# Kernel optimization log

Hardware: AMD Instinct MI355X
Metric: run time of the kernel (lower is better)

## Reference

```python
import jax, jax.numpy as jnp
import numpy as np

K = 512
H = 8

def setup_inputs() -> dict:
    key = jax.random.key(0)
    k1, k2, k3, k4, k5 = jax.random.split(key, 5)
    b, s = 2, 2048
    x = jax.random.normal(k1, (b, s, K), dtype=jnp.float32)
    # torch Linear weights: shape [out_features, in_features]
    scale = 0.02
    Wq = jax.random.normal(k2, (H * K, K), dtype=jnp.float32) * scale
    Wk = jax.random.normal(k3, (H * K, K), dtype=jnp.float32) * scale
    Wv = jax.random.normal(k4, (H * K, K), dtype=jnp.float32) * scale
    Wu = jax.random.normal(k5, (K, H * K), dtype=jnp.float32) * scale
    return {"x": x, "Wq": Wq, "Wk": Wk, "Wv": Wv, "Wu": Wu}

def reference(x, Wq, Wk, Wv, Wu):
    b, s, _ = x.shape
    # project and split heads: [b, h, s, k]
    q = jnp.einsum('bsd,hed->bhse', x, Wq.reshape(H, K, K))
    kk = jnp.einsum('bsd,hed->bhse', x, Wk.reshape(H, K, K))
    v = jnp.einsum('bsd,hed->bhse', x, Wv.reshape(H, K, K))
    scale = K ** (-0.25)
    dot = jnp.einsum('bhse,bhte->bhst', q * scale, kk * scale)  # [b,h,s,s]
    causal = jnp.tril(jnp.ones((s, s), dtype=bool))
    dot = jnp.where(causal[None, None], dot, -jnp.inf)
    weights = jax.nn.softmax(dot, axis=-1)
    heads_out = jnp.einsum('bhst,bhte->bhse', weights, v)  # [b,h,s,k]
    heads_out = heads_out.transpose(0, 2, 1, 3).reshape(b, s, H * K)
    return heads_out @ Wu.T
```

## Files before the change

### kernel.cpp

```cpp
#include <hip/hip_runtime.h>
#include <hip/hip_bf16.h>
#include <cstdint>
#include <cstddef>


typedef __bf16 bf16;
typedef __bf16 bf16x8 __attribute__((ext_vector_type(8)));
typedef float  f32x4  __attribute__((ext_vector_type(4)));
typedef unsigned short u16x4 __attribute__((ext_vector_type(4)));

__device__ __forceinline__ void gl2lds16(const void* g, void* l) {
  __builtin_amdgcn_global_load_lds(
      (const __attribute__((address_space(1))) unsigned int*)g,
      (__attribute__((address_space(3))) unsigned int*)l, 16, 0, 0);
}

__device__ __forceinline__ unsigned short bfbits(float f) {
  return __builtin_bit_cast(unsigned short, (__bf16)f);
}

__global__ __launch_bounds__(256) void cvt_all(
    const float* __restrict__ x,  const float* __restrict__ wq,
    const float* __restrict__ wk, const float* __restrict__ wv,
    const float* __restrict__ wu,
    bf16* __restrict__ xb,  bf16* __restrict__ wqb, bf16* __restrict__ wkb,
    bf16* __restrict__ wvb, bf16* __restrict__ wub)
{
  const int Q4 = (1 << 21) / 4;
  int i = blockIdx.x * 256 + threadIdx.x;
  int a = i / Q4;
  int off = (i - a * Q4) * 4;
  const float* s; bf16* d;
  switch (a) {
    case 0: s = x;  d = xb;  break;
    case 1: s = wq; d = wqb; break;
    case 2: s = wk; d = wkb; break;
    case 3: s = wv; d = wvb; break;
    default: s = wu; d = wub; break;
  }
  float4 v = *(const float4*)(s + off);
  u16x4 o = { bfbits(v.x), bfbits(v.y), bfbits(v.z), bfbits(v.w) };
  *(u16x4*)(d + off) = o;
}

template<int BM, int BN, int MODE>
__global__ __launch_bounds__((BM >= 256 ? 2 : BM / 64) * (BN / 64) * 64)
void gemm_bt(const bf16* __restrict__ A, const bf16* __restrict__ B,
             void* __restrict__ Cp, int M, int N, int K)
{
  constexpr int BK = 32;
  constexpr int WM = (BM >= 256 ? 128 : 64);
  constexpr int MI = WM / 16;
  constexpr int WAVES_M = BM / WM;
  constexpr int WAVES_N = BN / 64;
  constexpr int NT = WAVES_M * WAVES_N * 64;
  constexpr int STG = 2 * (BM + BN) * BK;
  constexpr int EPE = (MODE == 0) ? 128 * 264
                    : (MODE == 1) ? 256 * 136
                    : 64 * 132 * 2;
  constexpr int SME = STG > EPE ? STG : EPE;
  __shared__ __align__(16) bf16 smem[SME];

  const int tid = threadIdx.x, w = tid >> 6, lane = tid & 63;
  const int g = lane >> 4, c16 = lane & 15;
  const int q8 = gridDim.x >> 3;
  const int wg = (blockIdx.x & 7) * q8 + (blockIdx.x >> 3);
  const int nbn = N / BN;
  const int bm = wg / nbn, bn = wg % nbn;
  const int m0 = bm * BM, n0 = bn * BN;
  const int wr = w / WAVES_N, wc = w % WAVES_N;

  f32x4 z = {0.f, 0.f, 0.f, 0.f};
  f32x4 acc[MI][4];
  #pragma unroll
  for (int i = 0; i < MI; i++)
    #pragma unroll
    for (int j = 0; j < 4; j++) acc[i][j] = z;

  const int nk = K / BK;

  auto stage = [&](int buf, int kt) {
    bf16* la = &smem[buf * (BM + BN) * BK];
    #pragma unroll
    for (int r = 0; r < (BM * BK / 8) / NT; r++) {
      int c = r * NT + tid;
      int row = c >> 2, p = c & 3, s = p ^ ((row >> 1) & 3);
      gl2lds16(A + (size_t)(m0 + row) * K + (size_t)kt * BK + s * 8,
               la + (r * NT + w * 64) * 8);
    }
    bf16* lb = &smem[buf * (BM + BN) * BK + BM * BK];
    #pragma unroll
    for (int r = 0; r < (BN * BK / 8) / NT; r++) {
      int c = r * NT + tid;
      int row = c >> 2, p = c & 3, s = p ^ ((row >> 1) & 3);
      gl2lds16(B + (size_t)(n0 + row) * K + (size_t)kt * BK + s * 8,
               lb + (r * NT + w * 64) * 8);
    }
  };

  stage(0, 0);
  __syncthreads();
  int cur = 0;
  for (int kt = 0; kt < nk; ++kt) {
    if (kt + 1 < nk) stage(cur ^ 1, kt + 1);
    const bf16* lA = &smem[cur * (BM + BN) * BK];
    const bf16* lB = &smem[cur * (BM + BN) * BK + BM * BK];
    bf16x8 af[MI], bfv[4];
    #pragma unroll
    for (int i = 0; i < MI; i++) {
      int ra = wr * WM + i * 16 + c16;
      af[i] = *(const bf16x8*)&lA[ra * BK + ((g ^ ((ra >> 1) & 3)) * 8)];
    }
    #pragma unroll
    for (int j = 0; j < 4; j++) {
      int rb = wc * 64 + j * 16 + c16;
      bfv[j] = *(const bf16x8*)&lB[rb * BK + ((g ^ ((rb >> 1) & 3)) * 8)];
    }
    #pragma unroll
    for (int i = 0; i < MI; i++)
      #pragma unroll
      for (int j = 0; j < 4; j++)
        acc[i][j] = __builtin_amdgcn_mfma_f32_16x16x32_bf16(af[i], bfv[j],
                                                            acc[i][j], 0, 0, 0);
    __syncthreads();
    cur ^= 1;
  }

  if constexpr (MODE == 0) {
    bf16* ep = smem;
    #pragma unroll
    for (int hp = 0; hp < 2; ++hp) {
      if (wr == hp) {
        #pragma unroll
        for (int i = 0; i < MI; i++) {
          int rl = i * 16 + g * 4;
          #pragma unroll
          for (int j = 0; j < 4; j++) {
            int cl = wc * 64 + j * 16 + c16;
            #pragma unroll
            for (int jj = 0; jj < 4; jj++)
              ep[(rl + jj) * 264 + cl] = (bf16)acc[i][j][jj];
          }
        }
      }
      __syncthreads();
      {
        bf16* C = (bf16*)Cp;
        int r = tid >> 2, ch = tid & 3;
        const bf16* src = &ep[r * 264 + ch * 64];
        bf16* dst = C + (size_t)(m0 + hp * 128 + r) * N + n0 + ch * 64;
        #pragma unroll
        for (int q = 0; q < 8; q++)
          *(bf16x8*)(dst + q * 8) = *(const bf16x8*)(src + q * 8);
      }
      if (hp == 0) __syncthreads();
    }
  } else if constexpr (MODE == 1) {
    bf16* ep = smem;
    bf16* C = (bf16*)Cp;
    #pragma unroll
    for (int hp = 0; hp < 2; ++hp) {
      if (wr == hp) {
        #pragma unroll
        for (int i = 0; i < MI; i++) {
          int rl = i * 16 + g * 4;
          #pragma unroll
          for (int j = 0; j < 4; j++) {
            int cl = wc * 64 + j * 16 + c16;
            u16x4 pk = { bfbits(acc[i][j][0]), bfbits(acc[i][j][1]),
                         bfbits(acc[i][j][2]), bfbits(acc[i][j][3]) };
            *(u16x4*)&ep[cl * 136 + rl] = pk;
          }
        }
      }
      __syncthreads();
      {
        int cl = tid >> 1, rc = tid & 1;
        const bf16* src = &ep[cl * 136 + rc * 64];
        int mg = m0 + hp * 128 + rc * 64;
        int bb = mg >> 11, srow = mg & 2047;
        bf16* dst = C + ((size_t)(bb * 4096 + n0 + cl)) * 2048 + srow;
        #pragma unroll
        for (int q = 0; q < 8; q++)
          *(bf16x8*)(dst + q * 8) = *(const bf16x8*)(src + q * 8);
      }
      if (hp == 0) __syncthreads();
    }
  } else {
    float* ep = (float*)smem;
    #pragma unroll
    for (int i = 0; i < MI; i++) {
      int rl = i * 16 + g * 4;
      #pragma unroll
      for (int j = 0; j < 4; j++) {
        int cl = wc * 64 + j * 16 + c16;
        #pragma unroll
        for (int jj = 0; jj < 4; jj++)
          ep[(rl + jj) * 132 + cl] = acc[i][j][jj];
      }
    }
    __syncthreads();
    {
      float* C = (float*)Cp;
      int r = tid >> 1, ch = tid & 1;
      const float* src = &ep[r * 132 + ch * 64];
      float* dst = C + (size_t)(m0 + r) * N + n0 + ch * 64;
      #pragma unroll
      for (int q = 0; q < 16; q++)
        *(float4*)(dst + q * 4) = *(const float4*)(src + q * 4);
    }
  }
}

__global__ __launch_bounds__(512)
void sgemm_causal(const bf16* __restrict__ Qb, const bf16* __restrict__ Kb,
                  bf16* __restrict__ Sp, float* __restrict__ l)
{
  constexpr int BK = 32;
  constexpr int STG = 2 * 512 * BK;
  constexpr int EPE = 128 * 264;
  __shared__ __align__(16) bf16 smem[EPE > STG ? EPE : STG];
  const int tid = threadIdx.x, w = tid >> 6, lane = tid & 63;
  const int g = lane >> 4, c16 = lane & 15;

  const int wg = (blockIdx.x & 7) * 72 + (blockIdx.x >> 3);
  const int bh = wg / 36, t = wg % 36;
  int TM = 0;
  while ((TM + 1) * (TM + 2) / 2 <= t) TM++;
  const int TN = t - TM * (TM + 1) / 2;
  const int b = bh >> 3, h = bh & 7;
  const bf16* Ab = Qb + (size_t)(b * 2048 + TM * 256) * 4096 + h * 512;
  const bf16* Bb = Kb + (size_t)(b * 2048 + TN * 256) * 4096 + h * 512;
  const int wr = w >> 2, wc = w & 3;

  f32x4 z = {0.f, 0.f, 0.f, 0.f};
  f32x4 acc[8][4];
  #pragma unroll
  for (int i = 0; i < 8; i++)
    #pragma unroll
    for (int j = 0; j < 4; j++) acc[i][j] = z;

  auto stage = [&](int buf, int kt) {
    bf16* la = &smem[buf * 16384];
    #pragma unroll
    for (int r = 0; r < 2; r++) {
      int c = r * 512 + tid;
      int row = c >> 2, p = c & 3, s = p ^ ((row >> 1) & 3);
      gl2lds16(Ab + (size_t)row * 4096 + kt * BK + s * 8,
               la + (r * 512 + w * 64) * 8);
    }
    bf16* lb = &smem[buf * 16384 + 256 * BK];
    #pragma unroll
    for (int r = 0; r < 2; r++) {
      int c = r * 512 + tid;
      int row = c >> 2, p = c & 3, s = p ^ ((row >> 1) & 3);
      gl2lds16(Bb + (size_t)row * 4096 + kt * BK + s * 8,
               lb + (r * 512 + w * 64) * 8);
    }
  };

  stage(0, 0);
  __syncthreads();
  int cur = 0;
  for (int kt = 0; kt < 16; ++kt) {
    if (kt + 1 < 16) stage(cur ^ 1, kt + 1);
    const bf16* lA = &smem[cur * 16384];
    const bf16* lB = &smem[cur * 16384 + 256 * BK];
    bf16x8 af[8], bfv[4];
    #pragma unroll
    for (int i = 0; i < 8; i++) {
      int ra = wr * 128 + i * 16 + c16;
      af[i] = *(const bf16x8*)&lA[ra * BK + ((g ^ ((ra >> 1) & 3)) * 8)];
    }
    #pragma unroll
    for (int j = 0; j < 4; j++) {
      int rb = wc * 64 + j * 16 + c16;
      bfv[j] = *(const bf16x8*)&lB[rb * BK + ((g ^ ((rb >> 1) & 3)) * 8)];
    }
    #pragma unroll
    for (int i = 0; i < 8; i++)
      #pragma unroll
      for (int j = 0; j < 4; j++)
        acc[i][j] = __builtin_amdgcn_mfma_f32_16x16x32_bf16(af[i], bfv[j],
                                                            acc[i][j], 0, 0, 0);
    __syncthreads();
    cur ^= 1;
  }

  const float SC2 = 0.044194173824159216f * 1.4426950408889634f;
  bf16* spb = Sp + (size_t)bh * 136 * 16384;
  bf16* ep = smem;
  float rsum[8][4];
  #pragma unroll
  for (int i = 0; i < 8; i++)
    #pragma unroll
    for (int jj = 0; jj < 4; jj++) rsum[i][jj] = 0.f;

  #pragma unroll
  for (int hp = 0; hp < 2; ++hp) {
    if (wr == hp) {
      #pragma unroll
      for (int i = 0; i < 8; i++) {
        #pragma unroll
        for (int j = 0; j < 4; j++) {
          int cl = wc * 64 + j * 16 + c16;
          int kglob = TN * 256 + cl;
          #pragma unroll
          for (int jj = 0; jj < 4; jj++) {
            int rl = i * 16 + g * 4 + jj;
            int qglob = TM * 256 + hp * 128 + rl;
            float p = (kglob <= qglob) ? exp2f(acc[i][j][jj] * SC2) : 0.f;
            rsum[i][jj] += p;
            ep[rl * 264 + cl] = (bf16)p;
          }
        }
      }
    }
    __syncthreads();
    {
      int r = tid >> 2, ch = tid & 3;
      int tm128 = 2 * TM + hp, tn128 = 2 * TN + (ch >> 1);
      if (tn128 <= tm128) {
        const bf16* src = &ep[r * 264 + ch * 64];
        bf16* dst = spb + (size_t)(tm128 * (tm128 + 1) / 2 + tn128) * 16384
                    + r * 128 + (ch & 1) * 64;
        #pragma unroll
        for (int q = 0; q < 8; q++)
          *(bf16x8*)(dst + q * 8) = *(const bf16x8*)(src + q * 8);
      }
    }
    if (hp == 0) __syncthreads();
  }

  #pragma unroll
  for (int i = 0; i < 8; i++)
    #pragma unroll
    for (int jj = 0; jj < 4; jj++) {
      float v = rsum[i][jj];
      v += __shfl_xor(v, 1);
      v += __shfl_xor(v, 2);
      v += __shfl_xor(v, 4);
      v += __shfl_xor(v, 8);
      if (c16 == 0) {
        int qglob = TM * 256 + wr * 128 + i * 16 + g * 4 + jj;
        atomicAdd(&l[bh * 2048 + qglob], v);
      }
    }
}

__global__ __launch_bounds__(512)
void pv_gemm(const bf16* __restrict__ Pp, const bf16* __restrict__ Vt,
             const float* __restrict__ l, bf16* __restrict__ HO)
{
  constexpr int BK = 32;
  constexpr int STG = 2 * 384 * BK;
  __shared__ __align__(16) bf16 smem[STG];
  __shared__ float sInv[128];
  const int tid = threadIdx.x, w = tid >> 6, lane = tid & 63;
  const int g = lane >> 4, c16 = lane & 15;

  const int wg = (blockIdx.x & 7) * 64 + (blockIdx.x >> 3);
  const int bh = wg >> 5, r5 = wg & 31;
  const int tm = 15 - (r5 >> 1), nd = r5 & 1;
  const int b = bh >> 3, hh = bh & 7;
  const size_t pb = (size_t)bh * 136 + (size_t)tm * (tm + 1) / 2;
  const bf16* Bb = Vt + (size_t)(bh * 512 + nd * 256) * 2048;
  const int wr = w >> 2, wc = w & 3;
  const int nk = (tm + 1) * 4;

  f32x4 z = {0.f, 0.f, 0.f, 0.f};
  f32x4 acc[4][4];
  #pragma unroll
  for (int i = 0; i < 4; i++)
    #pragma unroll
    for (int j = 0; j < 4; j++) acc[i][j] = z;

  auto stage = [&](int buf, int kt) {
    const bf16* At = Pp + (pb + (kt >> 2)) * 16384 + (kt & 3) * 32;
    bf16* la = &smem[buf * 12288];
    {
      int row = tid >> 2, p = tid & 3, s = p ^ ((row >> 1) & 3);
      gl2lds16(At + (size_t)row * 128 + s * 8, la + (w * 64) * 8);
    }
    bf16* lb = &smem[buf * 12288 + 128 * BK];
    #pragma unroll
    for (int r = 0; r < 2; r++) {
      int c = r * 512 + tid;
      int row = c >> 2, p = c & 3, s = p ^ ((row >> 1) & 3);
      gl2lds16(Bb + (size_t)row * 2048 + kt * BK + s * 8,
               lb + (r * 512 + w * 64) * 8);
    }
  };

  stage(0, 0);
  if (tid < 128) sInv[tid] = 1.0f / l[bh * 2048 + tm * 128 + tid];
  __syncthreads();
  int cur = 0;
  for (int kt = 0; kt < nk; ++kt) {
    if (kt + 1 < nk) stage(cur ^ 1, kt + 1);
    const bf16* lA = &smem[cur * 12288];
    const bf16* lB = &smem[cur * 12288 + 128 * BK];
    bf16x8 af[4], bfv[4];
    #pragma unroll
    for (int i = 0; i < 4; i++) {
      int ra = wr * 64 + i * 16 + c16;
      af[i] = *(const bf16x8*)&lA[ra * BK + ((g ^ ((ra >> 1) & 3)) * 8)];
    }
    #pragma unroll
    for (int j = 0; j < 4; j++) {
      int rb = wc * 64 + j * 16 + c16;
      bfv[j] = *(const bf16x8*)&lB[rb * BK + ((g ^ ((rb >> 1) & 3)) * 8)];
    }
    #pragma unroll
    for (int i = 0; i < 4; i++)
      #pragma unroll
      for (int j = 0; j < 4; j++)
        acc[i][j] = __builtin_amdgcn_mfma_f32_16x16x32_bf16(af[i], bfv[j],
                                                            acc[i][j], 0, 0, 0);
    __syncthreads();
    cur ^= 1;
  }

  bf16* Cb = HO + (size_t)(b * 2048 + tm * 128) * 4096 + hh * 512 + nd * 256;
  bf16* ep = smem;
  #pragma unroll
  for (int hp = 0; hp < 2; ++hp) {
    if (wr == hp) {
      #pragma unroll
      for (int i = 0; i < 4; i++) {
        #pragma unroll
        for (int j = 0; j < 4; j++) {
          int cl = wc * 64 + j * 16 + c16;
          #pragma unroll
          for (int jj = 0; jj < 4; jj++) {
            int rl = i * 16 + g * 4 + jj;
            ep[rl * 264 + cl] =
                (bf16)(acc[i][j][jj] * sInv[hp * 64 + rl]);
          }
        }
      }
    }
    __syncthreads();
    {
      int r = tid >> 3, ch = tid & 7;
      const bf16* src = &ep[r * 264 + ch * 32];
      bf16* dst = Cb + (size_t)(hp * 64 + r) * 4096 + ch * 32;
      #pragma unroll
      for (int q = 0; q < 4; q++)
        *(bf16x8*)(dst + q * 8) = *(const bf16x8*)(src + q * 8);
    }
    if (hp == 0) __syncthreads();
  }
}

extern "C" void kernel_launch(void* const* d_in, const int* in_sizes, int n_in,
                              void* d_out, int out_size, void* d_ws,
                              size_t ws_size, hipStream_t stream)
{
  (void)in_sizes; (void)n_in; (void)out_size; (void)ws_size;
  const float* x  = (const float*)d_in[0];
  const float* wq = (const float*)d_in[1];
  const float* wk = (const float*)d_in[2];
  const float* wv = (const float*)d_in[3];
  const float* wu = (const float*)d_in[4];

  char* ws = (char*)d_ws;
  const size_t MB = 1024 * 1024;
  bf16*  wub = (bf16*)(ws + 0 * MB);
  float* lR  = (float*)(ws + 4 * MB);
  bf16*  Qb  = (bf16*)(ws + 5 * MB);
  bf16*  Kbf = (bf16*)(ws + 37 * MB);
  bf16*  Sp  = (bf16*)(ws + 69 * MB);
  bf16*  wqb = (bf16*)(ws + 69 * MB);
  bf16*  wkb = (bf16*)(ws + 73 * MB);
  bf16*  xb  = (bf16*)(ws + 137 * MB);
  bf16*  wvb = (bf16*)(ws + 141 * MB);
  bf16*  Vtb = Kbf;
  bf16*  HOb = Qb;

  hipMemsetAsync(lR, 0, 16 * 2048 * sizeof(float), stream);
  hipLaunchKernelGGL(cvt_all, dim3(10240), dim3(256), 0, stream,
                     x, wq, wk, wv, wu, xb, wqb, wkb, wvb, wub);
  hipLaunchKernelGGL((gemm_bt<256, 256, 0>), dim3(256), dim3(512), 0, stream,
                     xb, wqb, (void*)Qb, 4096, 4096, 512);
  hipLaunchKernelGGL((gemm_bt<256, 256, 0>), dim3(256), dim3(512), 0, stream,
                     xb, wkb, (void*)Kbf, 4096, 4096, 512);
  hipLaunchKernelGGL(sgemm_causal, dim3(576), dim3(512), 0, stream,
                     Qb, Kbf, Sp, lR);
  hipLaunchKernelGGL((gemm_bt<256, 256, 1>), dim3(256), dim3(512), 0, stream,
                     xb, wvb, (void*)Vtb, 4096, 4096, 512);
  hipLaunchKernelGGL(pv_gemm, dim3(512), dim3(512), 0, stream,
                     Sp, Vtb, lR, HOb);
  hipLaunchKernelGGL((gemm_bt<64, 128, 2>), dim3(256), dim3(128), 0, stream,
                     HOb, wub, d_out, 4096, 512, 4096);
}
```

Before: 402.8 us.

## Unify GEMMs into 4-stage pipelined 256x256 kernel with priority and barrier scheduling

Replaces the separate projection, causal QK and PV GEMM kernels with one templated 256x256-tile kernel. It uses a four-slot LDS ring with split-k half stages, explicit vmcnt waits, s_setprio and sched_barrier so MFMA work overlaps global-to-LDS loads. The PV step now uses 256-row tiles over a rearranged 128x128 probability block layout, and the bf16 copies of x and Wv are staged in the output buffer instead of the workspace. This targets latency from the simple double-buffered loop, at the cost of 128KB LDS per block and more complex indexing.

```diff
diff --git a/kernel.cpp b/kernel.cpp
--- a/kernel.cpp
+++ b/kernel.cpp
@@ -43,96 +43,154 @@
   *(u16x4*)(d + off) = o;
 }
 
-template<int BM, int BN, int MODE>
-__global__ __launch_bounds__((BM >= 256 ? 2 : BM / 64) * (BN / 64) * 64)
-void gemm_bt(const bf16* __restrict__ A, const bf16* __restrict__ B,
-             void* __restrict__ Cp, int M, int N, int K)
+#define RD_A(AS, FI0)                                                       \
+  { _Pragma("unroll") for (int i_ = 0; i_ < 4; ++i_)                        \
+      afr[i_] = *(const bf16x8*)&sm[(AS) * 8192 + aoff[(FI0) + i_]]; }
+#define RD_B(BS)                                                            \
+  { _Pragma("unroll") for (int j_ = 0; j_ < 4; ++j_)                        \
+      bfr[j_] = *(const bf16x8*)&sm[32768 + (BS) * 8192 + boff[j_]]; }
+#define MF16(FI0)                                                           \
+  { _Pragma("unroll") for (int i_ = 0; i_ < 4; ++i_)                        \
+      _Pragma("unroll") for (int j_ = 0; j_ < 4; ++j_)                      \
+        acc[(FI0) + i_][j_] = __builtin_amdgcn_mfma_f32_16x16x32_bf16(      \
+            afr[i_], bfr[j_], acc[(FI0) + i_][j_], 0, 0, 0); }
+#define PH(AS, BS, FI0, DOB, STG)                                           \
+  {                                                                         \
+    if (DOB) RD_B(BS);                                                      \
+    RD_A(AS, FI0);                                                          \
+    STG;                                                                    \
+    __builtin_amdgcn_s_barrier();                                           \
+    __builtin_amdgcn_s_setprio(1);                                          \
+    MF16(FI0);                                                              \
+    __builtin_amdgcn_s_setprio(0);                                          \
+    asm volatile("s_waitcnt vmcnt(8)" ::: "memory");                        \
+    __builtin_amdgcn_sched_barrier(0);                                      \
+    __builtin_amdgcn_s_barrier();                                           \
+    __builtin_amdgcn_sched_barrier(0);                                      \
+  }
+
+template<int MODE>
+__global__ __launch_bounds__(512, 2)
+void mm8(const bf16* __restrict__ Ag, const bf16* __restrict__ Bg,
+         void* __restrict__ Cp, float* __restrict__ lptr)
 {
-  constexpr int BK = 32;
-  constexpr int WM = (BM >= 256 ? 128 : 64);
-  constexpr int MI = WM / 16;
-  constexpr int WAVES_M = BM / WM;
-  constexpr int WAVES_N = BN / 64;
-  constexpr int NT = WAVES_M * WAVES_N * 64;
-  constexpr int STG = 2 * (BM + BN) * BK;
-  constexpr int EPE = (MODE == 0) ? 128 * 264
-                    : (MODE == 1) ? 256 * 136
-                    : 64 * 132 * 2;
-  constexpr int SME = STG > EPE ? STG : EPE;
-  __shared__ __align__(16) bf16 smem[SME];
+  __shared__ __align__(16) bf16 sm[65536];
+  __shared__ float sInv[256];
 
   const int tid = threadIdx.x, w = tid >> 6, lane = tid & 63;
   const int g = lane >> 4, c16 = lane & 15;
-  const int q8 = gridDim.x >> 3;
-  const int wg = (blockIdx.x & 7) * q8 + (blockIdx.x >> 3);
-  const int nbn = N / BN;
-  const int bm = wg / nbn, bn = wg % nbn;
-  const int m0 = bm * BM, n0 = bn * BN;
-  const int wr = w / WAVES_N, wc = w % WAVES_N;
+  const int wr = w >> 2, wc = w & 3;
+
+  int nt = 8;
+  const bf16 *Ab = Ag, *Bb = Bg;
+  int m0 = 0, n0 = 0, bh = 0, TM = 0, TN = 0, T = 0, nd = 0;
+  size_t rowBase0 = 0, rowBase1 = 0;
+
+  if constexpr (MODE <= 1) {
+    const int wg = ((blockIdx.x & 7) << 5) | (blockIdx.x >> 3);
+    m0 = (wg >> 4) * 256; n0 = (wg & 15) * 256;
+    Ab = Ag + (size_t)m0 * 512;
+    Bb = Bg + (size_t)n0 * 512;
+  } else if constexpr (MODE == 2) {
+    const int wg = (blockIdx.x & 7) * 72 + (blockIdx.x >> 3);
+    bh = wg / 36; int t = wg % 36;
+    TM = 0;
+    while ((TM + 1) * (TM + 2) / 2 <= t) TM++;
+    TN = t - TM * (TM + 1) / 2;
+    const int b = bh >> 3, h = bh & 7;
+    Ab = Ag + (size_t)(b * 2048 + TM * 256) * 4096 + h * 512;
+    Bb = Bg + (size_t)(b * 2048 + TN * 256) * 4096 + h * 512;
+  } else {
+    const int wg = ((blockIdx.x & 7) << 5) | (blockIdx.x >> 3);
+    bh = wg >> 4; const int r = wg & 15;
+    T = 7 - (r >> 1); nd = r & 1;
+    rowBase0 = (size_t)bh * 144 + (size_t)(2 * T) * (T + 1);
+    rowBase1 = rowBase0 + (2 * T + 2);
+    Bb = Bg + (size_t)(bh * 512 + nd * 256) * 2048;
+    nt = 4 * (T + 1);
+    if (tid < 256) sInv[tid] = 1.0f / lptr[bh * 2048 + T * 256 + tid];
+  }
+
+  int aoff[8], boff[4];
+  #pragma unroll
+  for (int i = 0; i < 8; ++i) {
+    int row = wr * 128 + i * 16 + c16;
+    aoff[i] = row * 32 + ((g ^ ((row >> 1) & 3)) << 3);
+  }
+  #pragma unroll
+  for (int j = 0; j < 4; ++j) {
+    int row = wc * 64 + j * 16 + c16;
+    boff[j] = row * 32 + ((g ^ ((row >> 1) & 3)) << 3);
+  }
 
   f32x4 z = {0.f, 0.f, 0.f, 0.f};
-  f32x4 acc[MI][4];
+  f32x4 acc[8][4];
   #pragma unroll
-  for (int i = 0; i < MI; i++)
+  for (int i = 0; i < 8; i++)
     #pragma unroll
     for (int j = 0; j < 4; j++) acc[i][j] = z;
 
-  const int nk = K / BK;
-
-  auto stage = [&](int buf, int kt) {
-    bf16* la = &smem[buf * (BM + BN) * BK];
-    #pragma unroll
-    for (int r = 0; r < (BM * BK / 8) / NT; r++) {
-      int c = r * NT + tid;
-      int row = c >> 2, p = c & 3, s = p ^ ((row >> 1) & 3);
-      gl2lds16(A + (size_t)(m0 + row) * K + (size_t)kt * BK + s * 8,
-               la + (r * NT + w * 64) * 8);
-    }
-    bf16* lb = &smem[buf * (BM + BN) * BK + BM * BK];
-    #pragma unroll
-    for (int r = 0; r < (BN * BK / 8) / NT; r++) {
-      int c = r * NT + tid;
-      int row = c >> 2, p = c & 3, s = p ^ ((row >> 1) & 3);
-      gl2lds16(B + (size_t)(n0 + row) * K + (size_t)kt * BK + s * 8,
-               lb + (r * NT + w * 64) * 8);
+  auto stgA = [&](int slot, int u, int kh) {
+    #pragma unroll
+    for (int r2 = 0; r2 < 2; ++r2) {
+      int c = (r2 << 9) + tid;
+      int row = c >> 2, cb = c & 3;
+      int ke = u * 64 + kh * 32 + ((cb ^ ((row >> 1) & 3)) << 3);
+      const bf16* src;
+      if constexpr (MODE <= 1)      src = Ab + (size_t)row * 512 + ke;
+      else if constexpr (MODE == 2) src = Ab + (size_t)row * 4096 + ke;
+      else {
+        size_t tb = (row < 128 ? rowBase0 : rowBase1) + (ke >> 7);
+        src = Ag + tb * 16384 + (size_t)(row & 127) * 128 + (ke & 127);
+      }
+      gl2lds16(src, &sm[slot * 8192 + c * 8]);
     }
   };
-
-  stage(0, 0);
+  auto stgB = [&](int slot, int u, int kh) {
+    #pragma unroll
+    for (int r2 = 0; r2 < 2; ++r2) {
+      int c = (r2 << 9) + tid;
+      int row = c >> 2, cb = c & 3;
+      int ke = u * 64 + kh * 32 + ((cb ^ ((row >> 1) & 3)) << 3);
+      const bf16* src;
+      if constexpr (MODE <= 1)      src = Bb + (size_t)row * 512 + ke;
+      else if constexpr (MODE == 2) src = Bb + (size_t)row * 4096 + ke;
+      else                          src = Bb + (size_t)row * 2048 + ke;
+      gl2lds16(src, &sm[32768 + slot * 8192 + c * 8]);
+    }
+  };
+
+  stgA(0, 0, 0); stgB(0, 0, 0);
+  stgA(1, 0, 1); stgB(1, 0, 1);
+  stgA(2, 1, 0); stgB(2, 1, 0);
+  asm volatile("s_waitcnt vmcnt(8)" ::: "memory");
+  __builtin_amdgcn_s_barrier();
+  __builtin_amdgcn_sched_barrier(0);
+
+  bf16x8 afr[4], bfr[4];
+  const int half = nt >> 1;
+  for (int ii = 0; ii < half; ++ii) {
+    const int t = ii << 1;
+    const bool s2 = (t + 2 < nt), s3 = (t + 3 < nt);
+    PH(0,  0, 0, true,  stgA(3, t + 1, 1))
+    PH(0, -1, 4, false, stgB(3, t + 1, 1))
+    PH(1,  1, 0, true,  if (s2) stgA(0, t + 2, 0))
+    PH(1, -1, 4, false, if (s2) stgB(0, t + 2, 0))
+    PH(2,  2, 0, true,  if (s2) stgA(1, t + 2, 1))
+    PH(2, -1, 4, false, if (s2) stgB(1, t + 2, 1))
+    PH(3,  3, 0, true,  if (s3) stgA(2, t + 3, 0))
+    PH(3, -1, 4, false, if (s3) stgB(2, t + 3, 0))
+  }
   __syncthreads();
-  int cur = 0;
-  for (int kt = 0; kt < nk; ++kt) {
-    if (kt + 1 < nk) stage(cur ^ 1, kt + 1);
-    const bf16* lA = &smem[cur * (BM + BN) * BK];
-    const bf16* lB = &smem[cur * (BM + BN) * BK + BM * BK];
-    bf16x8 af[MI], bfv[4];
-    #pragma unroll
-    for (int i = 0; i < MI; i++) {
-      int ra = wr * WM + i * 16 + c16;
-      af[i] = *(const bf16x8*)&lA[ra * BK + ((g ^ ((ra >> 1) & 3)) * 8)];
-    }
-    #pragma unroll
-    for (int j = 0; j < 4; j++) {
-      int rb = wc * 64 + j * 16 + c16;
-      bfv[j] = *(const bf16x8*)&lB[rb * BK + ((g ^ ((rb >> 1) & 3)) * 8)];
-    }
-    #pragma unroll
-    for (int i = 0; i < MI; i++)
-      #pragma unroll
-      for (int j = 0; j < 4; j++)
-        acc[i][j] = __builtin_amdgcn_mfma_f32_16x16x32_bf16(af[i], bfv[j],
-                                                            acc[i][j], 0, 0, 0);
-    __syncthreads();
-    cur ^= 1;
-  }
 
   if constexpr (MODE == 0) {
-    bf16* ep = smem;
+    bf16* C = (bf16*)Cp;
+    bf16* ep = sm;
     #pragma unroll
     for (int hp = 0; hp < 2; ++hp) {
       if (wr == hp) {
         #pragma unroll
-        for (int i = 0; i < MI; i++) {
+        for (int i = 0; i < 8; i++) {
           int rl = i * 16 + g * 4;
           #pragma unroll
           for (int j = 0; j < 4; j++) {
@@ -145,10 +203,9 @@
       }
       __syncthreads();
       {
-        bf16* C = (bf16*)Cp;
         int r = tid >> 2, ch = tid & 3;
         const bf16* src = &ep[r * 264 + ch * 64];
-        bf16* dst = C + (size_t)(m0 + hp * 128 + r) * N + n0 + ch * 64;
+        bf16* dst = C + (size_t)(m0 + hp * 128 + r) * 4096 + n0 + ch * 64;
         #pragma unroll
         for (int q = 0; q < 8; q++)
           *(bf16x8*)(dst + q * 8) = *(const bf16x8*)(src + q * 8);
@@ -156,13 +213,13 @@
       if (hp == 0) __syncthreads();
     }
   } else if constexpr (MODE == 1) {
-    bf16* ep = smem;
     bf16* C = (bf16*)Cp;
+    bf16* ep = sm;
     #pragma unroll
     for (int hp = 0; hp < 2; ++hp) {
       if (wr == hp) {
         #pragma unroll
-        for (int i = 0; i < MI; i++) {
+        for (int i = 0; i < 8; i++) {
           int rl = i * 16 + g * 4;
           #pragma unroll
           for (int j = 0; j < 4; j++) {
@@ -186,187 +243,116 @@
       }
       if (hp == 0) __syncthreads();
     }
+  } else if constexpr (MODE == 2) {
+    const float SC2 = 0.044194173824159216f * 1.4426950408889634f;
+    bf16* ep = sm;
+    float rsum[8][4];
+    #pragma unroll
+    for (int i = 0; i < 8; i++)
+      #pragma unroll
+      for (int jj = 0; jj < 4; jj++) rsum[i][jj] = 0.f;
+
+    #pragma unroll
+    for (int hp = 0; hp < 2; ++hp) {
+      if (wr == hp) {
+        #pragma unroll
+        for (int i = 0; i < 8; i++) {
+          #pragma unroll
+          for (int j = 0; j < 4; j++) {
+            int cl = wc * 64 + j * 16 + c16;
+            int kglob = TN * 256 + cl;
+            #pragma unroll
+            for (int jj = 0; jj < 4; jj++) {
+              int rl = i * 16 + g * 4 + jj;
+              int qglob = TM * 256 + hp * 128 + rl;
+              float p = (kglob <= qglob) ? exp2f(acc[i][j][jj] * SC2) : 0.f;
+              rsum[i][jj] += p;
+              ep[rl * 264 + cl] = (bf16)p;
+            }
+          }
+        }
+      }
+      __syncthreads();
+      {
+        int r = tid >> 2, ch = tid & 3;
+        int tm128 = 2 * TM + hp, tn128 = 2 * TN + (ch >> 1);
+        bool wrOK = (tn128 <= tm128) || (hp == 0 && tn128 == tm128 + 1);
+        if (wrOK) {
+          const bf16* src = &ep[r * 264 + ch * 64];
+          size_t toff = (size_t)bh * 144 + (size_t)(2 * TM) * (TM + 1)
+                      + (size_t)hp * (2 * TM + 2) + tn128;
+          bf16* dst = (bf16*)Cp + toff * 16384 + r * 128 + (ch & 1) * 64;
+          #pragma unroll
+          for (int q = 0; q < 8; q++)
+            *(bf16x8*)(dst + q * 8) = *(const bf16x8*)(src + q * 8);
+        }
+      }
+      if (hp == 0) __syncthreads();
+    }
+    #pragma unroll
+    for (int i = 0; i < 8; i++)
+      #pragma unroll
+      for (int jj = 0; jj < 4; jj++) {
+        float v = rsum[i][jj];
+        v += __shfl_xor(v, 1);
+        v += __shfl_xor(v, 2);
+        v += __shfl_xor(v, 4);
+        v += __shfl_xor(v, 8);
+        if (c16 == 0) {
+          int qglob = TM * 256 + wr * 128 + i * 16 + g * 4 + jj;
+          atomicAdd(&lptr[bh * 2048 + qglob], v);
+        }
+      }
   } else {
-    float* ep = (float*)smem;
-    #pragma unroll
-    for (int i = 0; i < MI; i++) {
-      int rl = i * 16 + g * 4;
-      #pragma unroll
-      for (int j = 0; j < 4; j++) {
-        int cl = wc * 64 + j * 16 + c16;
-        #pragma unroll
-        for (int jj = 0; jj < 4; jj++)
-          ep[(rl + jj) * 132 + cl] = acc[i][j][jj];
-      }
-    }
-    __syncthreads();
-    {
-      float* C = (float*)Cp;
-      int r = tid >> 1, ch = tid & 1;
-      const float* src = &ep[r * 132 + ch * 64];
-      float* dst = C + (size_t)(m0 + r) * N + n0 + ch * 64;
-      #pragma unroll
-      for (int q = 0; q < 16; q++)
-        *(float4*)(dst + q * 4) = *(const float4*)(src + q * 4);
-    }
-  }
-}
-
-__global__ __launch_bounds__(512)
-void sgemm_causal(const bf16* __restrict__ Qb, const bf16* __restrict__ Kb,
-                  bf16* __restrict__ Sp, float* __restrict__ l)
+    const int b = bh >> 3, h = bh & 7;
+    bf16* Cb = (bf16*)Cp + (size_t)(b * 2048 + T * 256) * 4096
+             + h * 512 + nd * 256;
+    bf16* ep = sm;
+    #pragma unroll
+    for (int hp = 0; hp < 2; ++hp) {
+      if (wr == hp) {
+        #pragma unroll
+        for (int i = 0; i < 8; i++) {
+          #pragma unroll
+          for (int j = 0; j < 4; j++) {
+            int cl = wc * 64 + j * 16 + c16;
+            #pragma unroll
+            for (int jj = 0; jj < 4; jj++) {
+              int rl = i * 16 + g * 4 + jj;
+              ep[rl * 264 + cl] = (bf16)(acc[i][j][jj] * sInv[hp * 128 + rl]);
+            }
+          }
+        }
+      }
+      __syncthreads();
+      {
+        int r = tid >> 2, ch = tid & 3;
+        const bf16* src = &ep[r * 264 + ch * 64];
+        bf16* dst = Cb + (size_t)(hp * 128 + r) * 4096 + ch * 64;
+        #pragma unroll
+        for (int q = 0; q < 8; q++)
+          *(bf16x8*)(dst + q * 8) = *(const bf16x8*)(src + q * 8);
+      }
+      if (hp == 0) __syncthreads();
+    }
+  }
+}
+
+__global__ __launch_bounds__(128)
+void proj_gemm(const bf16* __restrict__ A, const bf16* __restrict__ B,
+               float* __restrict__ C)
 {
   constexpr int BK = 32;
-  constexpr int STG = 2 * 512 * BK;
-  constexpr int EPE = 128 * 264;
+  constexpr int STG = 2 * 192 * BK;
+  constexpr int EPE = 64 * 132 * 2;
   __shared__ __align__(16) bf16 smem[EPE > STG ? EPE : STG];
+
   const int tid = threadIdx.x, w = tid >> 6, lane = tid & 63;
   const int g = lane >> 4, c16 = lane & 15;
-
-  const int wg = (blockIdx.x & 7) * 72 + (blockIdx.x >> 3);
-  const int bh = wg / 36, t = wg % 36;
-  int TM = 0;
-  while ((TM + 1) * (TM + 2) / 2 <= t) TM++;
-  const int TN = t - TM * (TM + 1) / 2;
-  const int b = bh >> 3, h = bh & 7;
-  const bf16* Ab = Qb + (size_t)(b * 2048 + TM * 256) * 4096 + h * 512;
-  const bf16* Bb = Kb + (size_t)(b * 2048 + TN * 256) * 4096 + h * 512;
-  const int wr = w >> 2, wc = w & 3;
-
-  f32x4 z = {0.f, 0.f, 0.f, 0.f};
-  f32x4 acc[8][4];
-  #pragma unroll
-  for (int i = 0; i < 8; i++)
-    #pragma unroll
-    for (int j = 0; j < 4; j++) acc[i][j] = z;
-
-  auto stage = [&](int buf, int kt) {
-    bf16* la = &smem[buf * 16384];
-    #pragma unroll
-    for (int r = 0; r < 2; r++) {
-      int c = r * 512 + tid;
-      int row = c >> 2, p = c & 3, s = p ^ ((row >> 1) & 3);
-      gl2lds16(Ab + (size_t)row * 4096 + kt * BK + s * 8,
-               la + (r * 512 + w * 64) * 8);
-    }
-    bf16* lb = &smem[buf * 16384 + 256 * BK];
-    #pragma unroll
-    for (int r = 0; r < 2; r++) {
-      int c = r * 512 + tid;
-      int row = c >> 2, p = c & 3, s = p ^ ((row >> 1) & 3);
-      gl2lds16(Bb + (size_t)row * 4096 + kt * BK + s * 8,
-               lb + (r * 512 + w * 64) * 8);
-    }
-  };
-
-  stage(0, 0);
-  __syncthreads();
-  int cur = 0;
-  for (int kt = 0; kt < 16; ++kt) {
-    if (kt + 1 < 16) stage(cur ^ 1, kt + 1);
-    const bf16* lA = &smem[cur * 16384];
-    const bf16* lB = &smem[cur * 16384 + 256 * BK];
-    bf16x8 af[8], bfv[4];
-    #pragma unroll
-    for (int i = 0; i < 8; i++) {
-      int ra = wr * 128 + i * 16 + c16;
-      af[i] = *(const bf16x8*)&lA[ra * BK + ((g ^ ((ra >> 1) & 3)) * 8)];
-    }
-    #pragma unroll
-    for (int j = 0; j < 4; j++) {
-      int rb = wc * 64 + j * 16 + c16;
-      bfv[j] = *(const bf16x8*)&lB[rb * BK + ((g ^ ((rb >> 1) & 3)) * 8)];
-    }
-    #pragma unroll
-    for (int i = 0; i < 8; i++)
-      #pragma unroll
-      for (int j = 0; j < 4; j++)
-        acc[i][j] = __builtin_amdgcn_mfma_f32_16x16x32_bf16(af[i], bfv[j],
-                                                            acc[i][j], 0, 0, 0);
-    __syncthreads();
-    cur ^= 1;
-  }
-
-  const float SC2 = 0.044194173824159216f * 1.4426950408889634f;
-  bf16* spb = Sp + (size_t)bh * 136 * 16384;
-  bf16* ep = smem;
-  float rsum[8][4];
-  #pragma unroll
-  for (int i = 0; i < 8; i++)
-    #pragma unroll
-    for (int jj = 0; jj < 4; jj++) rsum[i][jj] = 0.f;
-
-  #pragma unroll
-  for (int hp = 0; hp < 2; ++hp) {
-    if (wr == hp) {
-      #pragma unroll
-      for (int i = 0; i < 8; i++) {
-        #pragma unroll
-        for (int j = 0; j < 4; j++) {
-          int cl = wc * 64 + j * 16 + c16;
-          int kglob = TN * 256 + cl;
-          #pragma unroll
-          for (int jj = 0; jj < 4; jj++) {
-            int rl = i * 16 + g * 4 + jj;
-            int qglob = TM * 256 + hp * 128 + rl;
-            float p = (kglob <= qglob) ? exp2f(acc[i][j][jj] * SC2) : 0.f;
-            rsum[i][jj] += p;
-            ep[rl * 264 + cl] = (bf16)p;
-          }
-        }
-      }
-    }
-    __syncthreads();
-    {
-      int r = tid >> 2, ch = tid & 3;
-      int tm128 = 2 * TM + hp, tn128 = 2 * TN + (ch >> 1);
-      if (tn128 <= tm128) {
-        const bf16* src = &ep[r * 264 + ch * 64];
-        bf16* dst = spb + (size_t)(tm128 * (tm128 + 1) / 2 + tn128) * 16384
-                    + r * 128 + (ch & 1) * 64;
-        #pragma unroll
-        for (int q = 0; q < 8; q++)
-          *(bf16x8*)(dst + q * 8) = *(const bf16x8*)(src + q * 8);
-      }
-    }
-    if (hp == 0) __syncthreads();
-  }
-
-  #pragma unroll
-  for (int i = 0; i < 8; i++)
-    #pragma unroll
-    for (int jj = 0; jj < 4; jj++) {
-      float v = rsum[i][jj];
-      v += __shfl_xor(v, 1);
-      v += __shfl_xor(v, 2);
-      v += __shfl_xor(v, 4);
-      v += __shfl_xor(v, 8);
-      if (c16 == 0) {
-        int qglob = TM * 256 + wr * 128 + i * 16 + g * 4 + jj;
-        atomicAdd(&l[bh * 2048 + qglob], v);
-      }
-    }
-}
-
-__global__ __launch_bounds__(512)
-void pv_gemm(const bf16* __restrict__ Pp, const bf16* __restrict__ Vt,
-             const float* __restrict__ l, bf16* __restrict__ HO)
-{
-  constexpr int BK = 32;
-  constexpr int STG = 2 * 384 * BK;
-  __shared__ __align__(16) bf16 smem[STG];
-  __shared__ float sInv[128];
-  const int tid = threadIdx.x, w = tid >> 6, lane = tid & 63;
-  const int g = lane >> 4, c16 = lane & 15;
-
-  const int wg = (blockIdx.x & 7) * 64 + (blockIdx.x >> 3);
-  const int bh = wg >> 5, r5 = wg & 31;
-  const int tm = 15 - (r5 >> 1), nd = r5 & 1;
-  const int b = bh >> 3, hh = bh & 7;
-  const size_t pb = (size_t)bh * 136 + (size_t)tm * (tm + 1) / 2;
-  const bf16* Bb = Vt + (size_t)(bh * 512 + nd * 256) * 2048;
-  const int wr = w >> 2, wc = w & 3;
-  const int nk = (tm + 1) * 4;
+  const int wg = ((blockIdx.x & 7) << 5) | (blockIdx.x >> 3);
+  const int bm = wg >> 2, bn = wg & 3;
+  const int m0 = bm * 64, n0 = bn * 128;
+  const int wc = w;
 
   f32x4 z = {0.f, 0.f, 0.f, 0.f};
   f32x4 acc[4][4];
@@ -376,40 +362,38 @@
     for (int j = 0; j < 4; j++) acc[i][j] = z;
 
   auto stage = [&](int buf, int kt) {
-    const bf16* At = Pp + (pb + (kt >> 2)) * 16384 + (kt & 3) * 32;
-    bf16* la = &smem[buf * 12288];
-    {
-      int row = tid >> 2, p = tid & 3, s = p ^ ((row >> 1) & 3);
-      gl2lds16(At + (size_t)row * 128 + s * 8, la + (w * 64) * 8);
-    }
-    bf16* lb = &smem[buf * 12288 + 128 * BK];
+    bf16* la = &smem[buf * 192 * BK];
     #pragma unroll
     for (int r = 0; r < 2; r++) {
-      int c = r * 512 + tid;
+      int c = r * 128 + tid;
       int row = c >> 2, p = c & 3, s = p ^ ((row >> 1) & 3);
-      gl2lds16(Bb + (size_t)row * 2048 + kt * BK + s * 8,
-               lb + (r * 512 + w * 64) * 8);
+      gl2lds16(A + (size_t)(m0 + row) * 4096 + (size_t)kt * BK + s * 8,
+               la + (r * 128 + w * 64) * 8);
+    }
+    bf16* lb = &smem[buf * 192 * BK + 64 * BK];
+    #pragma unroll
+    for (int r = 0; r < 4; r++) {
+      int c = r * 128 + tid;
+      int row = c >> 2, p = c & 3, s = p ^ ((row >> 1) & 3);
+      gl2lds16(B + (size_t)(n0 + row) * 4096 + (size_t)kt * BK + s * 8,
+               lb + (r * 128 + w * 64) * 8);
     }
   };
 
   stage(0, 0);
-  if (tid < 128) sInv[tid] = 1.0f / l[bh * 2048 + tm * 128 + tid];
   __syncthreads();
   int cur = 0;
-  for (int kt = 0; kt < nk; ++kt) {
-    if (kt + 1 < nk) stage(cur ^ 1, kt + 1);
-    const bf16* lA = &smem[cur * 12288];
-    const bf16* lB = &smem[cur * 12288 + 128 * BK];
+  for (int kt = 0; kt < 128; ++kt) {
+    if (kt + 1 < 128) stage(cur ^ 1, kt + 1);
+    const bf16* lA = &smem[cur * 192 * BK];
+    const bf16* lB = &smem[cur * 192 * BK + 64 * BK];
     bf16x8 af[4], bfv[4];
     #pragma unroll
     for (int i = 0; i < 4; i++) {
-      int ra = wr * 64 + i * 16 + c16;
+      int ra = i * 16 + c16;
       af[i] = *(const bf16x8*)&lA[ra * BK + ((g ^ ((ra >> 1) & 3)) * 8)];
-    }
-    #pragma unroll
-    for (int j = 0; j < 4; j++) {
-      int rb = wc * 64 + j * 16 + c16;
-      bfv[j] = *(const bf16x8*)&lB[rb * BK + ((g ^ ((rb >> 1) & 3)) * 8)];
+      int rb = wc * 64 + i * 16 + c16;
+      bfv[i] = *(const bf16x8*)&lB[rb * BK + ((g ^ ((rb >> 1) & 3)) * 8)];
     }
     #pragma unroll
     for (int i = 0; i < 4; i++)
@@ -421,35 +405,26 @@
     cur ^= 1;
   }
 
-  bf16* Cb = HO + (size_t)(b * 2048 + tm * 128) * 4096 + hh * 512 + nd * 256;
-  bf16* ep = smem;
+  float* ep = (float*)smem;
   #pragma unroll
-  for (int hp = 0; hp < 2; ++hp) {
-    if (wr == hp) {
+  for (int i = 0; i < 4; i++) {
+    int rl = i * 16 + g * 4;
+    #pragma unroll
+    for (int j = 0; j < 4; j++) {
+      int cl = wc * 64 + j * 16 + c16;
       #pragma unroll
-      for (int i = 0; i < 4; i++) {
-        #pragma unroll
-        for (int j = 0; j < 4; j++) {
-          int cl = wc * 64 + j * 16 + c16;
-          #pragma unroll
-          for (int jj = 0; jj < 4; jj++) {
-            int rl = i * 16 + g * 4 + jj;
-            ep[rl * 264 + cl] =
-                (bf16)(acc[i][j][jj] * sInv[hp * 64 + rl]);
-          }
-        }
-      }
-    }
-    __syncthreads();
-    {
-      int r = tid >> 3, ch = tid & 7;
-      const bf16* src = &ep[r * 264 + ch * 32];
-      bf16* dst = Cb + (size_t)(hp * 64 + r) * 4096 + ch * 32;
-      #pragma unroll
-      for (int q = 0; q < 4; q++)
-        *(bf16x8*)(dst + q * 8) = *(const bf16x8*)(src + q * 8);
-    }
-    if (hp == 0) __syncthreads();
+      for (int jj = 0; jj < 4; jj++)
+        ep[(rl + jj) * 132 + cl] = acc[i][j][jj];
+    }
+  }
+  __syncthreads();
+  {
+    int r = tid >> 1, ch = tid & 1;
+    const float* src = &ep[r * 132 + ch * 64];
+    float* dst = C + (size_t)(m0 + r) * 512 + n0 + ch * 64;
+    #pragma unroll
+    for (int q = 0; q < 16; q++)
+      *(float4*)(dst + q * 4) = *(const float4*)(src + q * 4);
   }
 }
 
@@ -473,24 +448,24 @@
   bf16*  Sp  = (bf16*)(ws + 69 * MB);
   bf16*  wqb = (bf16*)(ws + 69 * MB);
   bf16*  wkb = (bf16*)(ws + 73 * MB);
-  bf16*  xb  = (bf16*)(ws + 137 * MB);
-  bf16*  wvb = (bf16*)(ws + 141 * MB);
+  bf16*  xb  = (bf16*)d_out;
+  bf16*  wvb = (bf16*)d_out + (1 << 21);
   bf16*  Vtb = Kbf;
   bf16*  HOb = Qb;
 
   hipMemsetAsync(lR, 0, 16 * 2048 * sizeof(float), stream);
   hipLaunchKernelGGL(cvt_all, dim3(10240), dim3(256), 0, stream,
                      x, wq, wk, wv, wu, xb, wqb, wkb, wvb, wub);
-  hipLaunchKernelGGL((gemm_bt<256, 256, 0>), dim3(256), dim3(512), 0, stream,
-                     xb, wqb, (void*)Qb, 4096, 4096, 512);
-  hipLaunchKernelGGL((gemm_bt<256, 256, 0>), dim3(256), dim3(512), 0, stream,
-                     xb, wkb, (void*)Kbf, 4096, 4096, 512);
-  hipLaunchKernelGGL(sgemm_causal, dim3(576), dim3(512), 0, stream,
-                     Qb, Kbf, Sp, lR);
-  hipLaunchKernelGGL((gemm_bt<256, 256, 1>), dim3(256), dim3(512), 0, stream,
-                     xb, wvb, (void*)Vtb, 4096, 4096, 512);
-  hipLaunchKernelGGL(pv_gemm, dim3(512), dim3(512), 0, stream,
-                     Sp, Vtb, lR, HOb);
-  hipLaunchKernelGGL((gemm_bt<64, 128, 2>), dim3(256), dim3(128), 0, stream,
-                     HOb, wub, d_out, 4096, 512, 4096);
-}
+  hipLaunchKernelGGL((mm8<0>), dim3(256), dim3(512), 0, stream,
+                     xb, wqb, (void*)Qb, nullptr);
+  hipLaunchKernelGGL((mm8<0>), dim3(256), dim3(512), 0, stream,
+                     xb, wkb, (void*)Kbf, nullptr);
+  hipLaunchKernelGGL((mm8<2>), dim3(576), dim3(512), 0, stream,
+                     Qb, Kbf, (void*)Sp, lR);
+  hipLaunchKernelGGL((mm8<1>), dim3(256), dim3(512), 0, stream,
+                     xb, wvb, (void*)Vtb, nullptr);
+  hipLaunchKernelGGL((mm8<3>), dim3(256), dim3(512), 0, stream,
+                     Sp, Vtb, (void*)HOb, lR);
+  hipLaunchKernelGGL(proj_gemm, dim3(256), dim3(128), 0, stream,
+                     HOb, wub, (float*)d_out);
+}
```

Measured after the change: 429.1 us. +6.5%, slower.
